# Optimization experiments

Measured on AMD Instinct MI355X. Metric: run time of the kernel, lower is better.

The kernel has to match this reference:

```python
import jax, jax.numpy as jnp
import numpy as np

N_NODES = 100000
N_EDGES = 1600000
F_IN = 128
F_HID = 16


def _gcn_conv(x, src, dst, W, b, n):
    # PyG GCNConv: x' = D^{-1/2} (A + I) D^{-1/2} (x W) + b
    h = x @ W                                   # [N, F_out] transform first (small F)
    deg = jax.ops.segment_sum(jnp.ones_like(dst, dtype=h.dtype), dst, num_segments=n)
    dinv = jnp.where(deg > 0, jax.lax.rsqrt(deg), 0.0)
    norm = dinv[src] * dinv[dst]                # [E+N] edge weights
    msg = h[src] * norm[:, None]                # gather + scale
    out = jax.ops.segment_sum(msg, dst, num_segments=n)  # scatter-add
    return out + b


def setup_inputs() -> dict:
    key = jax.random.key(0)
    k1, k2, k3, k4 = jax.random.split(key, 4)
    x = jax.random.normal(k1, (N_NODES, F_IN), dtype=jnp.float32)
    edge_index = jax.random.randint(k2, (2, N_EDGES), 0, N_NODES, dtype=jnp.int64)
    # Glorot-ish init for the two GCNConv weights
    W1 = jax.random.normal(k3, (F_IN, F_HID), dtype=jnp.float32) * (1.0 / np.sqrt(F_IN))
    b1 = jnp.zeros((F_HID,), dtype=jnp.float32)
    W2 = jax.random.normal(k4, (F_HID, F_IN), dtype=jnp.float32) * (1.0 / np.sqrt(F_HID))
    b2 = jnp.zeros((F_IN,), dtype=jnp.float32)
    return {"x": x, "edge_index": edge_index, "W1": W1, "b1": b1, "W2": W2, "b2": b2}


def reference(x, edge_index, W1, b1, W2, b2):
    n = x.shape[0]
    # add self-loops once (GCNConv default add_self_loops=True)
    loop = jnp.arange(n, dtype=edge_index.dtype)
    src = jnp.concatenate([edge_index[0], loop])
    dst = jnp.concatenate([edge_index[1], loop])
    h = _gcn_conv(x, src, dst, W1, b1, n)
    h = jax.nn.relu(h)
    out = _gcn_conv(h, src, dst, W2, b2, n)
    return out
```

## Files before the change

### kernel.cpp

```cpp
#include <hip/hip_runtime.h>
#include <hip/hip_fp16.h>


#define NN 100000
#define NE 1600000
#define FI 128
#define FH 16
#define CB 64
#define NB 1563
#define GC 128
#define CHUNK 12500

__device__ __forceinline__ float fc(const float4& v, int i) {
    return i == 0 ? v.x : i == 1 ? v.y : i == 2 ? v.z : v.w;
}

__global__ __launch_bounds__(256) void k_count(const int* __restrict__ dst,
                                               int* __restrict__ hist) {
    __shared__ int h[NB];
    for (int i = threadIdx.x; i < NB; i += 256) h[i] = 0;
    __syncthreads();
    int base = blockIdx.x * CHUNK;
    for (int i = base + threadIdx.x; i < base + CHUNK; i += 256)
        atomicAdd(&h[dst[i] >> 6], 1);
    __syncthreads();
    for (int b = threadIdx.x; b < NB; b += 256)
        hist[b * GC + blockIdx.x] = h[b];
}

__global__ __launch_bounds__(GC) void k_scan_blocks(int* __restrict__ hist,
                                                    int* __restrict__ totals) {
    __shared__ int s[GC];
    int tid = threadIdx.x;
    int v = hist[blockIdx.x * GC + tid];
    s[tid] = v;
    __syncthreads();
    #pragma unroll
    for (int off = 1; off < GC; off <<= 1) {
        int t = (tid >= off) ? s[tid - off] : 0;
        __syncthreads();
        s[tid] += t;
        __syncthreads();
    }
    hist[blockIdx.x * GC + tid] = s[tid] - v;
    if (tid == GC - 1) totals[blockIdx.x] = s[GC - 1];
}

__global__ __launch_bounds__(1024) void k_scan_buckets(const int* __restrict__ totals,
                                                       int* __restrict__ bucketStart,
                                                       int* __restrict__ rowStart) {
    __shared__ int s[1024];
    int tid = threadIdx.x;
    int i0 = 2 * tid, i1 = i0 + 1;
    int a = (i0 < NB) ? totals[i0] : 0;
    int b = (i1 < NB) ? totals[i1] : 0;
    s[tid] = a + b;
    __syncthreads();
    #pragma unroll
    for (int off = 1; off < 1024; off <<= 1) {
        int t = (tid >= off) ? s[tid - off] : 0;
        __syncthreads();
        s[tid] += t;
        __syncthreads();
    }
    int excl = s[tid] - (a + b);
    if (i0 < NB) bucketStart[i0] = excl;
    if (i1 < NB) bucketStart[i1] = excl + a;
    if (tid == 0) { bucketStart[NB] = NE; rowStart[NN] = NE; }
}

__global__ __launch_bounds__(GC) void k_addback(int* __restrict__ hist,
                                                const int* __restrict__ bucketStart) {
    hist[blockIdx.x * GC + threadIdx.x] += bucketStart[blockIdx.x];
}

__global__ __launch_bounds__(256) void k_scatter(const int* __restrict__ src,
                                                 const int* __restrict__ dst,
                                                 const int* __restrict__ hist,
                                                 int* __restrict__ packed) {
    __shared__ int cur[NB];
    for (int b = threadIdx.x; b < NB; b += 256)
        cur[b] = hist[b * GC + blockIdx.x];
    __syncthreads();
    int base = blockIdx.x * CHUNK;
    for (int i = base + threadIdx.x; i < base + CHUNK; i += 256) {
        int d = dst[i];
        int pos = atomicAdd(&cur[d >> 6], 1);
        packed[pos] = src[i] | ((d & 63) << 17);
    }
}

__global__ __launch_bounds__(256) void k_bsort(const int* __restrict__ packed,
                                               const int* __restrict__ bucketStart,
                                               int* __restrict__ csr,
                                               int* __restrict__ rowStart,
                                               float* __restrict__ dinv) {
    __shared__ int cnt[CB];
    __shared__ int rs[CB];
    __shared__ int cur[CB];
    if (threadIdx.x < CB) cnt[threadIdx.x] = 0;
    __syncthreads();
    int s0 = bucketStart[blockIdx.x], s1 = bucketStart[blockIdx.x + 1];
    for (int i = s0 + threadIdx.x; i < s1; i += 256)
        atomicAdd(&cnt[(packed[i] >> 17) & 63], 1);
    __syncthreads();
    if (threadIdx.x < CB) rs[threadIdx.x] = cnt[threadIdx.x];
    __syncthreads();
    #pragma unroll
    for (int off = 1; off < CB; off <<= 1) {
        int t = 0;
        if (threadIdx.x < CB && threadIdx.x >= off) t = rs[threadIdx.x - off];
        __syncthreads();
        if (threadIdx.x < CB) rs[threadIdx.x] += t;
        __syncthreads();
    }
    if (threadIdx.x < CB) {
        int start = s0 + rs[threadIdx.x] - cnt[threadIdx.x];
        cur[threadIdx.x] = start;
        int node = blockIdx.x * CB + threadIdx.x;
        if (node < NN) {
            rowStart[node] = start;
            dinv[node] = rsqrtf((float)(cnt[threadIdx.x] + 1));
        }
    }
    __syncthreads();
    for (int i = s0 + threadIdx.x; i < s1; i += 256) {
        int pk = packed[i];
        int pos = atomicAdd(&cur[(pk >> 17) & 63], 1);
        csr[pos] = pk & 131071;
    }
}

__global__ __launch_bounds__(256) void k_gemm1(const float* __restrict__ x,
                                               const float* __restrict__ W1,
                                               const float* __restrict__ dinv,
                                               __half2* __restrict__ g1) {
    __shared__ __align__(16) float w[FI * FH];
    float4* w4s = (float4*)w;
    w4s[threadIdx.x] = ((const float4*)W1)[threadIdx.x];
    w4s[threadIdx.x + 256] = ((const float4*)W1)[threadIdx.x + 256];
    __syncthreads();
    int fg = threadIdx.x & 3;
    int ng = threadIdx.x >> 2;
    int r0 = blockIdx.x * 256 + ng * 4;
    const float4* x4 = (const float4*)x;
    int rr[4]; bool val[4];
    #pragma unroll
    for (int i = 0; i < 4; ++i) {
        val[i] = (r0 + i < NN);
        rr[i] = val[i] ? r0 + i : NN - 1;
    }
    float acc[4][4];
    #pragma unroll
    for (int i = 0; i < 4; ++i)
        #pragma unroll
        for (int j = 0; j < 4; ++j) acc[i][j] = 0.f;
    #pragma unroll 2
    for (int k4 = 0; k4 < 32; ++k4) {
        float4 xv[4];
        #pragma unroll
        for (int i = 0; i < 4; ++i) xv[i] = x4[rr[i] * 32 + k4];
        #pragma unroll
        for (int kk = 0; kk < 4; ++kk) {
            float4 wv = w4s[(k4 * 4 + kk) * 4 + fg];
            #pragma unroll
            for (int i = 0; i < 4; ++i) {
                float xk = fc(xv[i], kk);
                acc[i][0] += xk * wv.x; acc[i][1] += xk * wv.y;
                acc[i][2] += xk * wv.z; acc[i][3] += xk * wv.w;
            }
        }
    }
    #pragma unroll
    for (int i = 0; i < 4; ++i) if (val[i]) {
        float dv = dinv[rr[i]];
        g1[rr[i] * 8 + fg * 2]     = __floats2half2_rn(acc[i][0] * dv, acc[i][1] * dv);
        g1[rr[i] * 8 + fg * 2 + 1] = __floats2half2_rn(acc[i][2] * dv, acc[i][3] * dv);
    }
}

template<bool RELU>
__global__ __launch_bounds__(256) void k_agg(const int* __restrict__ csr,
                                             const int* __restrict__ rowStart,
                                             const __half2* __restrict__ gin,
                                             const float* __restrict__ dinv,
                                             const float* __restrict__ b1,
                                             __half2* __restrict__ gh_out,
                                             float2* __restrict__ p2f) {
    int gid = blockIdx.x * 256 + threadIdx.x;
    int node = gid >> 3, c = gid & 7;
    if (node >= NN) return;
    int s0 = rowStart[node], s1 = rowStart[node + 1];
    float2 acc = __half22float2(gin[node * 8 + c]);
    int e = s0;
    for (; e + 3 < s1; e += 4) {
        int i0 = csr[e], i1 = csr[e + 1], i2 = csr[e + 2], i3 = csr[e + 3];
        float2 f0 = __half22float2(gin[i0 * 8 + c]);
        float2 f1 = __half22float2(gin[i1 * 8 + c]);
        float2 f2 = __half22float2(gin[i2 * 8 + c]);
        float2 f3 = __half22float2(gin[i3 * 8 + c]);
        acc.x += (f0.x + f1.x) + (f2.x + f3.x);
        acc.y += (f0.y + f1.y) + (f2.y + f3.y);
    }
    for (; e < s1; ++e) {
        float2 f = __half22float2(gin[csr[e] * 8 + c]);
        acc.x += f.x; acc.y += f.y;
    }
    float dv = dinv[node];
    if (RELU) {
        float2 bb = *(const float2*)(b1 + 2 * c);
        float vx = fmaxf(dv * acc.x + bb.x, 0.f) * dv;
        float vy = fmaxf(dv * acc.y + bb.y, 0.f) * dv;
        gh_out[node * 8 + c] = __floats2half2_rn(vx, vy);
    } else {
        p2f[node * 8 + c] = make_float2(dv * acc.x, dv * acc.y);
    }
}

__global__ __launch_bounds__(256) void k_gemm2(const float* __restrict__ p2s,
                                               const float* __restrict__ W2,
                                               const float* __restrict__ b2,
                                               float* __restrict__ out) {
    __shared__ __align__(16) float w[FH * FI];
    __shared__ __align__(16) float pst[FH][32];
    float4* w4s = (float4*)w;
    w4s[threadIdx.x] = ((const float4*)W2)[threadIdx.x];
    w4s[threadIdx.x + 256] = ((const float4*)W2)[threadIdx.x + 256];
    int base = blockIdx.x * 32;
    {
        int n = threadIdx.x >> 4, k = threadIdx.x & 15;
        int gn = base + n;
        pst[k][n] = (gn < NN) ? p2s[gn * 16 + k] : 0.f;
        n += 16; gn = base + n;
        pst[k][n] = (gn < NN) ? p2s[gn * 16 + k] : 0.f;
    }
    __syncthreads();
    int fg = threadIdx.x & 31;
    int ng = threadIdx.x >> 5;
    float4 bb = ((const float4*)b2)[fg];
    float acc[4][4];
    #pragma unroll
    for (int i = 0; i < 4; ++i) {
        acc[i][0] = bb.x; acc[i][1] = bb.y; acc[i][2] = bb.z; acc[i][3] = bb.w;
    }
    #pragma unroll
    for (int k = 0; k < FH; ++k) {
        float4 xk = *(float4*)&pst[k][ng * 4];
        float4 wv = w4s[k * 32 + fg];
        #pragma unroll
        for (int i = 0; i < 4; ++i) {
            float xv = fc(xk, i);
            acc[i][0] += xv * wv.x; acc[i][1] += xv * wv.y;
            acc[i][2] += xv * wv.z; acc[i][3] += xv * wv.w;
        }
    }
    #pragma unroll
    for (int i = 0; i < 4; ++i) {
        int gn = base + ng * 4 + i;
        if (gn < NN)
            ((float4*)out)[gn * 32 + fg] =
                make_float4(acc[i][0], acc[i][1], acc[i][2], acc[i][3]);
    }
}

extern "C" void kernel_launch(void* const* d_in, const int* in_sizes, int n_in,
                              void* d_out, int out_size, void* d_ws, size_t ws_size,
                              hipStream_t stream) {
    const float* x  = (const float*)d_in[0];
    const int*   ei = (const int*)d_in[1];
    const float* W1 = (const float*)d_in[2];
    const float* b1 = (const float*)d_in[3];
    const float* W2 = (const float*)d_in[4];
    const float* b2 = (const float*)d_in[5];
    float* out = (float*)d_out;

    const int* src = ei;
    const int* dst = ei + NE;

    int*   hist        = (int*)d_ws;
    int*   totals      = hist + NB * GC;
    int*   bucketStart = totals + NB;
    int*   rowStart    = bucketStart + NB + 1;
    float* dinv        = (float*)(rowStart + NN + 1);
    int*   csr         = (int*)(dinv + NN);
    int*   packed      = csr + NE;
    __half2* g1        = (__half2*)packed;
    __half2* g2        = g1 + NN * 8;
    float2*  p2f       = (float2*)(packed + NE);

    k_count       <<<GC, 256, 0, stream>>>(dst, hist);
    k_scan_blocks <<<NB, GC, 0, stream>>>(hist, totals);
    k_scan_buckets<<<1, 1024, 0, stream>>>(totals, bucketStart, rowStart);
    k_addback     <<<NB, GC, 0, stream>>>(hist, bucketStart);
    k_scatter     <<<GC, 256, 0, stream>>>(src, dst, hist, packed);
    k_bsort       <<<NB, 256, 0, stream>>>(packed, bucketStart, csr, rowStart, dinv);

    k_gemm1       <<<(NN + 255) / 256, 256, 0, stream>>>(x, W1, dinv, g1);
    k_agg<true>   <<<(NN * 8) / 256, 256, 0, stream>>>(csr, rowStart, g1, dinv, b1, g2, (float2*)nullptr);
    k_agg<false>  <<<(NN * 8) / 256, 256, 0, stream>>>(csr, rowStart, g2, dinv, b1, (__half2*)nullptr, p2f);
    k_gemm2       <<<(NN + 31) / 32, 256, 0, stream>>>((const float*)p2f, W2, b2, out);
}
```

Before: 235.8 us.

## Use more counting chunks, chunk-major histogram, fold bucket offset into scatter

After: 227.3 us. 3.6% less time.

```diff
diff --git a/kernel.cpp b/kernel.cpp
--- a/kernel.cpp
+++ b/kernel.cpp
@@ -8,8 +8,9 @@
 #define FH 16
 #define CB 64
 #define NB 1563
-#define GC 128
-#define CHUNK 12500
+#define GC 512
+#define CHUNK 3125
+#define SCB 16
 
 __device__ __forceinline__ float fc(const float4& v, int i) {
     return i == 0 ? v.x : i == 1 ? v.y : i == 2 ? v.z : v.w;
@@ -25,25 +26,48 @@
         atomicAdd(&h[dst[i] >> 6], 1);
     __syncthreads();
     for (int b = threadIdx.x; b < NB; b += 256)
-        hist[b * GC + blockIdx.x] = h[b];
-}
-
-__global__ __launch_bounds__(GC) void k_scan_blocks(int* __restrict__ hist,
-                                                    int* __restrict__ totals) {
-    __shared__ int s[GC];
-    int tid = threadIdx.x;
-    int v = hist[blockIdx.x * GC + tid];
-    s[tid] = v;
-    __syncthreads();
-    #pragma unroll
+        hist[blockIdx.x * NB + b] = h[b];
+}
+
+__global__ __launch_bounds__(256) void k_scan_chunks(int* __restrict__ hist,
+                                                     int* __restrict__ totals) {
+    __shared__ int s[GC * SCB];
+    int b0 = blockIdx.x * SCB;
+    int o[GC * SCB / 256];
+    #pragma unroll
+    for (int r = 0; r < GC * SCB / 256; ++r) {
+        int idx = r * 256 + threadIdx.x;
+        int c = idx >> 4, bl = idx & (SCB - 1), b = b0 + bl;
+        int v = (b < NB) ? hist[c * NB + b] : 0;
+        s[idx] = v;
+        o[r] = v;
+    }
+    __syncthreads();
     for (int off = 1; off < GC; off <<= 1) {
-        int t = (tid >= off) ? s[tid - off] : 0;
-        __syncthreads();
-        s[tid] += t;
-        __syncthreads();
-    }
-    hist[blockIdx.x * GC + tid] = s[tid] - v;
-    if (tid == GC - 1) totals[blockIdx.x] = s[GC - 1];
+        int t[GC * SCB / 256];
+        #pragma unroll
+        for (int r = 0; r < GC * SCB / 256; ++r) {
+            int idx = r * 256 + threadIdx.x;
+            int c = idx >> 4;
+            t[r] = (c >= off) ? s[idx - off * SCB] : 0;
+        }
+        __syncthreads();
+        #pragma unroll
+        for (int r = 0; r < GC * SCB / 256; ++r) {
+            int idx = r * 256 + threadIdx.x;
+            s[idx] += t[r];
+        }
+        __syncthreads();
+    }
+    #pragma unroll
+    for (int r = 0; r < GC * SCB / 256; ++r) {
+        int idx = r * 256 + threadIdx.x;
+        int c = idx >> 4, bl = idx & (SCB - 1), b = b0 + bl;
+        if (b < NB) {
+            hist[c * NB + b] = s[idx] - o[r];
+            if (c == GC - 1) totals[b] = s[idx];
+        }
+    }
 }
 
 __global__ __launch_bounds__(1024) void k_scan_buckets(const int* __restrict__ totals,
@@ -69,18 +93,14 @@
     if (tid == 0) { bucketStart[NB] = NE; rowStart[NN] = NE; }
 }
 
-__global__ __launch_bounds__(GC) void k_addback(int* __restrict__ hist,
-                                                const int* __restrict__ bucketStart) {
-    hist[blockIdx.x * GC + threadIdx.x] += bucketStart[blockIdx.x];
-}
-
 __global__ __launch_bounds__(256) void k_scatter(const int* __restrict__ src,
                                                  const int* __restrict__ dst,
                                                  const int* __restrict__ hist,
+                                                 const int* __restrict__ bucketStart,
                                                  int* __restrict__ packed) {
     __shared__ int cur[NB];
     for (int b = threadIdx.x; b < NB; b += 256)
-        cur[b] = hist[b * GC + blockIdx.x];
+        cur[b] = hist[blockIdx.x * NB + b] + bucketStart[b];
     __syncthreads();
     int base = blockIdx.x * CHUNK;
     for (int i = base + threadIdx.x; i < base + CHUNK; i += 256) {
@@ -277,22 +297,21 @@
     const int* src = ei;
     const int* dst = ei + NE;
 
-    int*   hist        = (int*)d_ws;
-    int*   totals      = hist + NB * GC;
+    int*   totals      = (int*)d_ws;
     int*   bucketStart = totals + NB;
     int*   rowStart    = bucketStart + NB + 1;
     float* dinv        = (float*)(rowStart + NN + 1);
     int*   csr         = (int*)(dinv + NN);
+    int*   hist        = csr;
     int*   packed      = csr + NE;
     __half2* g1        = (__half2*)packed;
     __half2* g2        = g1 + NN * 8;
     float2*  p2f       = (float2*)(packed + NE);
 
     k_count       <<<GC, 256, 0, stream>>>(dst, hist);
-    k_scan_blocks <<<NB, GC, 0, stream>>>(hist, totals);
+    k_scan_chunks <<<(NB + SCB - 1) / SCB, 256, 0, stream>>>(hist, totals);
     k_scan_buckets<<<1, 1024, 0, stream>>>(totals, bucketStart, rowStart);
-    k_addback     <<<NB, GC, 0, stream>>>(hist, bucketStart);
-    k_scatter     <<<GC, 256, 0, stream>>>(src, dst, hist, packed);
+    k_scatter     <<<GC, 256, 0, stream>>>(src, dst, hist, bucketStart, packed);
     k_bsort       <<<NB, 256, 0, stream>>>(packed, bucketStart, csr, rowStart, dinv);
 
     k_gemm1       <<<(NN + 255) / 256, 256, 0, stream>>>(x, W1, dinv, g1);
```
